# Optimization experiments

Measured on AMD Instinct MI355X. Metric: run time of the kernel, lower is better.

## Reference

```python
import jax, jax.numpy as jnp
import numpy as np

NL, D, DI, N, R, K = 4, 256, 512, 16, 16, 4  # layers, d_model, d_inner, d_state, dt_rank, conv kernel


def setup_inputs() -> dict:
    key = jax.random.key(0)
    ks = jax.random.split(key, 10)
    b, nc, nt = 8, 256, 64
    xc = jax.random.normal(ks[0], (b, nc, D), jnp.float32)
    xt = jax.random.normal(ks[1], (b, nt, D), jnp.float32)
    ln_g = jnp.ones((NL, D), jnp.float32)
    ln_b = jnp.zeros((NL, D), jnp.float32)
    W_in = jax.random.normal(ks[2], (NL, D, 2 * DI), jnp.float32) * (D ** -0.5)
    W_conv = jax.random.normal(ks[3], (NL, DI, 1, K), jnp.float32) * 0.2
    b_conv = jnp.zeros((NL, DI), jnp.float32)
    W_x = jax.random.normal(ks[4], (NL, DI, R + 2 * N), jnp.float32) * (DI ** -0.5)
    W_dt = jax.random.normal(ks[5], (NL, R, DI), jnp.float32) * (R ** -0.5)
    b_dt = jax.random.normal(ks[6], (NL, DI), jnp.float32) * 0.5 - 4.0  # softplus ~ 0.02
    A_log = jnp.broadcast_to(jnp.log(jnp.arange(1, N + 1, dtype=jnp.float32)), (NL, DI, N)).copy()
    Dp = jnp.ones((NL, DI), jnp.float32)
    W_out = jax.random.normal(ks[7], (NL, DI, D), jnp.float32) * (DI ** -0.5)
    return dict(xc=xc, xt=xt, ln_g=ln_g, ln_b=ln_b, W_in=W_in, W_conv=W_conv, b_conv=b_conv,
                W_x=W_x, W_dt=W_dt, b_dt=b_dt, A_log=A_log, Dp=Dp, W_out=W_out)


def _mamba_layer(x, g, beta, Wi, Wc, bc, Wx, Wdt, bdt, Alog, Dvec, Wo):
    # x: [B, L, D]; pre-LN residual Mamba-1 block
    mu = jnp.mean(x, axis=-1, keepdims=True)
    var = jnp.var(x, axis=-1, keepdims=True)
    h = (x - mu) * jax.lax.rsqrt(var + 1e-5) * g + beta
    xz = h @ Wi                              # [B, L, 2*DI]
    xp, z = xz[..., :DI], xz[..., DI:]
    # causal depthwise conv1d
    xcv = jax.lax.conv_general_dilated(xp.transpose(0, 2, 1), Wc, (1,), [(K - 1, 0)],
                                       feature_group_count=DI,
                                       dimension_numbers=('NCH', 'OIH', 'NCH'))
    xcv = jax.nn.silu(xcv.transpose(0, 2, 1) + bc)  # [B, L, DI]
    dbl = xcv @ Wx                           # [B, L, R+2N]
    dt = jax.nn.softplus(dbl[..., :R] @ Wdt + bdt)   # [B, L, DI]
    Bm = dbl[..., R:R + N]                   # [B, L, N]
    Cm = dbl[..., R + N:]                    # [B, L, N]
    A = -jnp.exp(Alog)                       # [DI, N]

    def step(hst, inp):
        x_t, dt_t, b_t, c_t = inp            # [B,DI],[B,DI],[B,N],[B,N]
        dA = jnp.exp(dt_t[:, :, None] * A)   # [B, DI, N]
        hst = dA * hst + (dt_t * x_t)[:, :, None] * b_t[:, None, :]
        return hst, jnp.einsum('bdn,bn->bd', hst, c_t)

    h0 = jnp.zeros((x.shape[0], DI, N), x.dtype)
    _, ys = jax.lax.scan(step, h0, (xcv.transpose(1, 0, 2), dt.transpose(1, 0, 2),
                                    Bm.transpose(1, 0, 2), Cm.transpose(1, 0, 2)))
    y = ys.transpose(1, 0, 2) + xcv * Dvec
    y = y * jax.nn.silu(z)
    return x + y @ Wo


def reference(xc, xt, ln_g, ln_b, W_in, W_conv, b_conv, W_x, W_dt, b_dt, A_log, Dp, W_out):
    b, nc, d = xc.shape
    nt = xt.shape[1]
    # replicate context per target token: [b*nt, nc+1, d]
    xr = jnp.broadcast_to(xc[:, None], (b, nt, nc, d)).reshape(b * nt, nc, d)
    x = jnp.concatenate([xr, xt.reshape(b * nt, 1, d)], axis=1)
    for i in range(NL):
        x = _mamba_layer(x, ln_g[i], ln_b[i], W_in[i], W_conv[i], b_conv[i],
                         W_x[i], W_dt[i], b_dt[i], A_log[i], Dp[i], W_out[i])
    return x[:, -1, :].reshape(b, nt, d)
```

## Files before the change

### kernel.cpp

```cpp
#include <hip/hip_runtime.h>
#include <hip/hip_bf16.h>

#define D_     256
#define TWO_DI 1024
#define DI_    512
#define NSTATE 16
#define RR     16
#define NDBL   48
#define BSEQ   8
#define NC     256
#define NCHUNK 16
#define CLEN   16
#define CTX    2048
#define TGT    512

typedef __attribute__((ext_vector_type(8))) short short8v;
typedef __attribute__((ext_vector_type(8))) unsigned short ushort8v;
typedef __attribute__((ext_vector_type(4))) float floatx4;

__device__ __forceinline__ float siluf(float x) { return x / (1.f + __expf(-x)); }
__device__ __forceinline__ float softplusf(float x) {
  return fmaxf(x, 0.f) + log1pf(__expf(-fabsf(x)));
}
__device__ __forceinline__ unsigned short f2bf(float x) {
  unsigned u = __float_as_uint(x);
  u += 0x7fffu + ((u >> 16) & 1u);
  return (unsigned short)(u >> 16);
}
__device__ __forceinline__ float bf2f(unsigned short b) {
  return __uint_as_float((unsigned)b << 16);
}

__global__ __launch_bounds__(256) void prep_all(
    const float* __restrict__ W_in, const float* __restrict__ W_o,
    const float* __restrict__ W_x, const float* __restrict__ Alog,
    unsigned short* __restrict__ Wint, unsigned short* __restrict__ Wot,
    unsigned short* __restrict__ Wxt, float* __restrict__ Aneg)
{
  __shared__ float tile[32][33];
  int b = blockIdx.x;
  const float* src; unsigned short* dst; int R, C, cx, ry;
  if (b < 1024) {
    int z = b >> 8, t = b & 255; cx = t & 31; ry = t >> 5; R = 256; C = 1024;
    src = W_in + (size_t)z * R * C; dst = Wint + (size_t)z * R * C;
  } else if (b < 1536) {
    int bb = b - 1024; int z = bb >> 7, t = bb & 127; cx = t & 7; ry = t >> 3; R = 512; C = 256;
    src = W_o + (size_t)z * R * C; dst = Wot + (size_t)z * R * C;
  } else if (b < 1664) {
    int bb = b - 1536; int z = bb >> 5, t = bb & 31; cx = t & 1; ry = t >> 1; R = 512; C = 48;
    src = W_x + (size_t)z * R * C; dst = Wxt + (size_t)z * R * C;
  } else {
    int i = (b - 1664) * 256 + threadIdx.x;
    if (i < 4 * DI_ * NSTATE) Aneg[i] = -__expf(Alog[i]);
    return;
  }
  int c0 = cx * 32, r0 = ry * 32;
  int tx = threadIdx.x & 31, ty = threadIdx.x >> 5;
#pragma unroll
  for (int i = 0; i < 4; ++i) {
    int r = r0 + ty + i * 8;
    tile[ty + i * 8][tx] = (r < R && c0 + tx < C) ? src[(size_t)r * C + c0 + tx] : 0.f;
  }
  __syncthreads();
#pragma unroll
  for (int i = 0; i < 4; ++i) {
    int c = c0 + ty + i * 8;
    if (c < C && r0 + tx < R)
      dst[(size_t)c * R + r0 + tx] = f2bf(tile[tx][ty + i * 8]);
  }
}

__device__ __forceinline__ void ln_body(int bx, const float* __restrict__ x,
    const float* __restrict__ g, const float* __restrict__ be,
    unsigned short* __restrict__ out, int rows)
{
  int wid = threadIdx.x >> 6, lane = threadIdx.x & 63;
  int row = bx * 4 + wid;
  if (row >= rows) return;
  const float4 v = *reinterpret_cast<const float4*>(&x[(size_t)row * D_ + lane * 4]);
  float s  = v.x + v.y + v.z + v.w;
  float sq = v.x * v.x + v.y * v.y + v.z * v.z + v.w * v.w;
#pragma unroll
  for (int off = 32; off; off >>= 1) {
    s  += __shfl_xor(s, off);
    sq += __shfl_xor(sq, off);
  }
  float mu   = s * (1.f / D_);
  float var  = sq * (1.f / D_) - mu * mu;
  float rstd = rsqrtf(var + 1e-5f);
  const float4 gv = *reinterpret_cast<const float4*>(&g[lane * 4]);
  const float4 bv = *reinterpret_cast<const float4*>(&be[lane * 4]);
  ushort4 o;
  o.x = f2bf((v.x - mu) * rstd * gv.x + bv.x);
  o.y = f2bf((v.y - mu) * rstd * gv.y + bv.y);
  o.z = f2bf((v.z - mu) * rstd * gv.z + bv.z);
  o.w = f2bf((v.w - mu) * rstd * gv.w + bv.w);
  *reinterpret_cast<ushort4*>(&out[(size_t)row * D_ + lane * 4]) = o;
}

__global__ __launch_bounds__(256) void ln_kern(const float* __restrict__ x,
    const float* __restrict__ g, const float* __restrict__ be,
    unsigned short* __restrict__ out, int rows)
{
  ln_body(blockIdx.x, x, g, be, out, rows);
}

__global__ __launch_bounds__(256) void fused_ln(
    const float* __restrict__ xA, const float* __restrict__ gA,
    const float* __restrict__ bA, unsigned short* __restrict__ oA,
    const float* __restrict__ xB, const float* __restrict__ gB,
    const float* __restrict__ bB, unsigned short* __restrict__ oB)
{
  if (blockIdx.x < CTX / 4) ln_body(blockIdx.x, xA, gA, bA, oA, CTX);
  else                      ln_body(blockIdx.x - CTX / 4, xB, gB, bB, oB, TGT);
}

template<int EPI>
__device__ __forceinline__ void gemm_body(
    unsigned short (*As)[72], unsigned short (*Bs)[72], int bx, int by,
    const unsigned short* __restrict__ A, const unsigned short* __restrict__ Bt,
    const float* __restrict__ resid, float* __restrict__ C, int M, int N, int K,
    const float* __restrict__ cconv, const float* __restrict__ Wc4,
    unsigned short* __restrict__ xcv_bf, float* __restrict__ zbuf)
{
  int tid = threadIdx.x;
  int n0 = bx * 64, m0 = by * 64;
  int w = tid >> 6, lane = tid & 63;
  int lr = lane & 15, kq = lane >> 4;
  int wr = w >> 1, wc = w & 1;
  int srow = tid >> 2, schunk = (tid & 3) * 16;
  const unsigned short* Ap = &A[(size_t)(m0 + srow) * K + schunk];
  const unsigned short* Bp = &Bt[(size_t)(n0 + srow) * K + schunk];
  ushort8v a0 = *reinterpret_cast<const ushort8v*>(Ap);
  ushort8v a1 = *reinterpret_cast<const ushort8v*>(Ap + 8);
  ushort8v b0 = *reinterpret_cast<const ushort8v*>(Bp);
  ushort8v b1 = *reinterpret_cast<const ushort8v*>(Bp + 8);
  floatx4 acc[2][2] = {};
  for (int k0 = 0; k0 < K; k0 += 64) {
    __syncthreads();
    *reinterpret_cast<ushort8v*>(&As[srow][schunk])     = a0;
    *reinterpret_cast<ushort8v*>(&As[srow][schunk + 8]) = a1;
    *reinterpret_cast<ushort8v*>(&Bs[srow][schunk])     = b0;
    *reinterpret_cast<ushort8v*>(&Bs[srow][schunk + 8]) = b1;
    __syncthreads();
    if (k0 + 64 < K) {
      a0 = *reinterpret_cast<const ushort8v*>(Ap + k0 + 64);
      a1 = *reinterpret_cast<const ushort8v*>(Ap + k0 + 72);
      b0 = *reinterpret_cast<const ushort8v*>(Bp + k0 + 64);
      b1 = *reinterpret_cast<const ushort8v*>(Bp + k0 + 72);
    }
#pragma unroll
    for (int ks = 0; ks < 2; ++ks) {
      short8v af[2], bf2v[2];
#pragma unroll
      for (int f = 0; f < 2; ++f)
        af[f] = *reinterpret_cast<const short8v*>(&As[wr * 32 + f * 16 + lr][ks * 32 + kq * 8]);
#pragma unroll
      for (int g2 = 0; g2 < 2; ++g2)
        bf2v[g2] = *reinterpret_cast<const short8v*>(&Bs[wc * 32 + g2 * 16 + lr][ks * 32 + kq * 8]);
#pragma unroll
      for (int f = 0; f < 2; ++f)
#pragma unroll
        for (int g2 = 0; g2 < 2; ++g2)
          acc[f][g2] = __builtin_amdgcn_mfma_f32_16x16x32_bf16(af[f], bf2v[g2], acc[f][g2], 0, 0, 0);
    }
  }
#pragma unroll
  for (int f = 0; f < 2; ++f)
#pragma unroll
    for (int g2 = 0; g2 < 2; ++g2) {
      int col = n0 + wc * 32 + g2 * 16 + lr;
#pragma unroll
      for (int r = 0; r < 4; ++r) {
        int row = m0 + wr * 32 + f * 16 + kq * 4 + r;
        float v = acc[f][g2][r];
        if (EPI == 0) {
          if (resid) v += resid[(size_t)row * N + col];
          C[(size_t)row * N + col] = v;
        } else {
          int b = row >> 6;
          if (col < DI_) {
            float sv = siluf(cconv[b * DI_ + col] + v * Wc4[col * 4 + 3]);
            xcv_bf[(size_t)row * DI_ + col] = f2bf(sv);
          } else {
            zbuf[(size_t)row * DI_ + (col - DI_)] = v;
          }
        }
      }
    }
}

template<int EPI>
__global__ __launch_bounds__(256) void gemm_bf16(
    const unsigned short* __restrict__ A, const unsigned short* __restrict__ Bt,
    const float* __restrict__ resid, float* __restrict__ C, int M, int N, int K,
    const float* __restrict__ cconv, const float* __restrict__ Wc4,
    unsigned short* __restrict__ xcv_bf, float* __restrict__ zbuf)
{
  __shared__ unsigned short As[64][72];
  __shared__ unsigned short Bs[64][72];
  gemm_body<EPI>(As, Bs, blockIdx.x, blockIdx.y, A, Bt, resid, C, M, N, K,
                 cconv, Wc4, xcv_bf, zbuf);
}

__global__ __launch_bounds__(256) void fused_gemm_in(
    const unsigned short* __restrict__ Aa, const unsigned short* __restrict__ Bta,
    float* __restrict__ Ca,
    const unsigned short* __restrict__ Ab, const unsigned short* __restrict__ Btb,
    const float* __restrict__ cconv, const float* __restrict__ Wc4,
    unsigned short* __restrict__ xcv_bf, float* __restrict__ zbuf)
{
  __shared__ unsigned short As[64][72];
  __shared__ unsigned short Bs[64][72];
  int f = blockIdx.x;
  if (f < 512)
    gemm_body<0>(As, Bs, f & 15, f >> 4, Aa, Bta, nullptr, Ca, CTX, TWO_DI, D_,
                 nullptr, nullptr, nullptr, nullptr);
  else {
    f -= 512;
    gemm_body<1>(As, Bs, f & 15, f >> 4, Ab, Btb, nullptr, nullptr, TGT, TWO_DI, D_,
                 cconv, Wc4, xcv_bf, zbuf);
  }
}

__device__ __forceinline__ void gemm_s_body(int bx, int by,
    const unsigned short* __restrict__ A, const unsigned short* __restrict__ Bt,
    const float* __restrict__ resid, float* __restrict__ C, int M, int N, int K)
{
  __shared__ unsigned short As[32][72];
  __shared__ unsigned short Bs[32][72];
  int tid = threadIdx.x;
  int n0 = bx * 32, m0 = by * 32;
  int w = tid >> 6, lane = tid & 63;
  int lr = lane & 15, kq = lane >> 4;
  int wr = w >> 1, wc = w & 1;
  int srow = tid >> 3, schunk = (tid & 7) * 8;
  const unsigned short* Ap = &A[(size_t)(m0 + srow) * K + schunk];
  const unsigned short* Bp = &Bt[(size_t)(n0 + srow) * K + schunk];
  ushort8v a0 = *reinterpret_cast<const ushort8v*>(Ap);
  ushort8v b0 = *reinterpret_cast<const ushort8v*>(Bp);
  floatx4 acc = {};
  for (int k0 = 0; k0 < K; k0 += 64) {
    __syncthreads();
    *reinterpret_cast<ushort8v*>(&As[srow][schunk]) = a0;
    *reinterpret_cast<ushort8v*>(&Bs[srow][schunk]) = b0;
    __syncthreads();
    if (k0 + 64 < K) {
      a0 = *reinterpret_cast<const ushort8v*>(Ap + k0 + 64);
      b0 = *reinterpret_cast<const ushort8v*>(Bp + k0 + 64);
    }
#pragma unroll
    for (int ks = 0; ks < 2; ++ks) {
      short8v af = *reinterpret_cast<const short8v*>(&As[wr * 16 + lr][ks * 32 + kq * 8]);
      short8v bf = *reinterpret_cast<const short8v*>(&Bs[wc * 16 + lr][ks * 32 + kq * 8]);
      acc = __builtin_amdgcn_mfma_f32_16x16x32_bf16(af, bf, acc, 0, 0, 0);
    }
  }
  int col = n0 + wc * 16 + lr;
#pragma unroll
  for (int r = 0; r < 4; ++r) {
    int row = m0 + wr * 16 + kq * 4 + r;
    float v = acc[r];
    if (resid) v += resid[(size_t)row * N + col];
    C[(size_t)row * N + col] = v;
  }
}

__global__ __launch_bounds__(256) void gemm_s(
    const unsigned short* __restrict__ A, const unsigned short* __restrict__ Bt,
    const float* __restrict__ resid, float* __restrict__ C, int M, int N, int K)
{
  gemm_s_body(blockIdx.x, blockIdx.y, A, Bt, resid, C, M, N, K);
}

__device__ __forceinline__ void conv_body(int blk,
    const float* __restrict__ xz, const float* __restrict__ Wc,
    const float* __restrict__ bc, const unsigned short* __restrict__ Wxt,
    const float* __restrict__ Wdt, const float* __restrict__ bdt,
    const float* __restrict__ Aneg,
    unsigned short* __restrict__ xcvb, float* __restrict__ dtb,
    float* __restrict__ dblg, float* __restrict__ cconv,
    float* __restrict__ Sb, float* __restrict__ Pb)
{
  __shared__ unsigned short xcs[16][528];
  __shared__ float dts_s[16][520];
  __shared__ float dbl_s[16][48];
  int seq = blk >> 4, ch = blk & 15;
  int tok0 = blk * 16;
  int tid = threadIdx.x;
#pragma unroll
  for (int hh = 0; hh < 2; ++hh) {
    int c = tid + hh * 256;
    float w0 = Wc[c * 4 + 0], w1 = Wc[c * 4 + 1], w2 = Wc[c * 4 + 2], w3 = Wc[c * 4 + 3];
    float bcv = bc[c];
    const float* xzs = &xz[(size_t)(seq * NC) * TWO_DI + c];
    for (int t = 0; t < 16; ++t) {
      int tl = ch * 16 + t;
      float acc = bcv + xzs[(size_t)tl * TWO_DI] * w3;
      if (tl >= 1) acc += xzs[(size_t)(tl - 1) * TWO_DI] * w2;
      if (tl >= 2) acc += xzs[(size_t)(tl - 2) * TWO_DI] * w1;
      if (tl >= 3) acc += xzs[(size_t)(tl - 3) * TWO_DI] * w0;
      unsigned short sv = f2bf(siluf(acc));
      xcs[t][c] = sv;
      xcvb[(size_t)(tok0 + t) * DI_ + c] = sv;
    }
    if (ch == 15)
      cconv[seq * DI_ + c] = bcv + xzs[(size_t)253 * TWO_DI] * w0
                                 + xzs[(size_t)254 * TWO_DI] * w1
                                 + xzs[(size_t)255 * TWO_DI] * w2;
  }
  __syncthreads();
  int w = tid >> 6, lane = tid & 63, lr = lane & 15, kq = lane >> 4;
  if (w < 3) {
    floatx4 acc = {};
#pragma unroll
    for (int kc = 0; kc < 16; ++kc) {
      short8v bb = *reinterpret_cast<const short8v*>(&Wxt[(size_t)(w * 16 + lr) * DI_ + kc * 32 + kq * 8]);
      short8v aa = *reinterpret_cast<const short8v*>(&xcs[lr][kc * 32 + kq * 8]);
      acc = __builtin_amdgcn_mfma_f32_16x16x32_bf16(aa, bb, acc, 0, 0, 0);
    }
#pragma unroll
    for (int r = 0; r < 4; ++r) {
      int t = kq * 4 + r, col = w * 16 + lr;
      dbl_s[t][col] = acc[r];
      dblg[(size_t)(tok0 + t) * NDBL + col] = acc[r];
    }
  }
  __syncthreads();
#pragma unroll
  for (int hh = 0; hh < 2; ++hh) {
    int c = tid + hh * 256;
    float wr_[16];
#pragma unroll
    for (int r = 0; r < 16; ++r) wr_[r] = Wdt[r * DI_ + c];
    float bv = bdt[c];
    for (int t = 0; t < 16; ++t) {
      float accd = bv;
#pragma unroll
      for (int r = 0; r < 16; ++r) accd += dbl_s[t][r] * wr_[r];
      float dtv = softplusf(accd);
      dts_s[t][c] = dtv;
      dtb[(size_t)(tok0 + t) * DI_ + c] = dtv;
    }
  }
  __syncthreads();
  int dl = tid >> 4, n = tid & 15;
  float Bt_r[16];
#pragma unroll
  for (int t = 0; t < 16; ++t) Bt_r[t] = dbl_s[t][RR + n];
  for (int dg = 0; dg < 32; ++dg) {
    int d = dg * 16 + dl;
    float A = Aneg[d * NSTATE + n];
    float h = 0.f, p = 1.f;
#pragma unroll
    for (int t = 0; t < 16; ++t) {
      float dtv = dts_s[t][d];
      float xv  = bf2f(xcs[t][d]);
      float dA  = __expf(dtv * A);
      h = fmaf(dA, h, dtv * xv * Bt_r[t]);
      p *= dA;
    }
    size_t o = ((size_t)blk * DI_ + d) * NSTATE + n;
    Sb[o] = h; Pb[o] = p;
  }
}

__global__ __launch_bounds__(256) void conv_dbl_part(
    const float* __restrict__ xz, const float* __restrict__ Wc,
    const float* __restrict__ bc, const unsigned short* __restrict__ Wxt,
    const float* __restrict__ Wdt, const float* __restrict__ bdt,
    const float* __restrict__ Aneg,
    unsigned short* __restrict__ xcvb, float* __restrict__ dtb,
    float* __restrict__ dblg, float* __restrict__ cconv,
    float* __restrict__ Sb, float* __restrict__ Pb)
{
  conv_body(blockIdx.x, xz, Wc, bc, Wxt, Wdt, bdt, Aneg, xcvb, dtb, dblg, cconv, Sb, Pb);
}

__device__ __forceinline__ void sf_body(int b,
    const float* __restrict__ dblg, const unsigned short* __restrict__ xcvb,
    const float* __restrict__ xz, const float* __restrict__ dtb,
    const float* __restrict__ Sb, const float* __restrict__ Pb,
    const float* __restrict__ Aneg, const float* __restrict__ Dp,
    unsigned short* __restrict__ yb, float* __restrict__ hstate)
{
  int dg = b & 31, sc = b >> 5;
  int seq = sc >> 4, chunk = sc & 15;
  int tid = threadIdx.x;
  int tt = tid >> 4, cc = tid & 15;
  int tok0 = sc * CLEN;
  __shared__ float dts[16][17], xs[16][17], zs[16][17], Bs[16][17], Cs[16][17], ys[16][17];
  dts[tt][cc] = dtb[(size_t)(tok0 + tt) * DI_ + dg * 16 + cc];
  xs[tt][cc]  = bf2f(xcvb[(size_t)(tok0 + tt) * DI_ + dg * 16 + cc]);
  zs[tt][cc]  = xz[(size_t)(tok0 + tt) * TWO_DI + DI_ + dg * 16 + cc];
  Bs[tt][cc]  = dblg[(size_t)(tok0 + tt) * NDBL + RR + cc];
  Cs[tt][cc]  = dblg[(size_t)(tok0 + tt) * NDBL + RR + NSTATE + cc];
  __syncthreads();
  int dl = tt, n = cc;
  int d = dg * 16 + dl;
  float A  = Aneg[d * NSTATE + n];
  float Dv = Dp[d];
  float Bn[16], Cn[16];
#pragma unroll
  for (int t = 0; t < CLEN; ++t) { Bn[t] = Bs[t][n]; Cn[t] = Cs[t][n]; }
  float h = 0.f;
  for (int c2 = 0; c2 < chunk; ++c2) {
    size_t o = ((size_t)(seq * NCHUNK + c2) * DI_ + d) * NSTATE + n;
    h = fmaf(Pb[o], h, Sb[o]);
  }
#pragma unroll
  for (int t = 0; t < CLEN; ++t) {
    float dtv = dts[t][dl];
    float xv  = xs[t][dl];
    float dA  = __expf(dtv * A);
    h = fmaf(dA, h, dtv * xv * Bn[t]);
    float p = h * Cn[t];
    p += __shfl_xor(p, 1); p += __shfl_xor(p, 2);
    p += __shfl_xor(p, 4); p += __shfl_xor(p, 8);
    if (n == 0) ys[t][dl] = (p + xv * Dv) * siluf(zs[t][dl]);
  }
  __syncthreads();
  yb[(size_t)(tok0 + tt) * DI_ + dg * 16 + cc] = f2bf(ys[tt][cc]);
  if (chunk == NCHUNK - 1)
    hstate[(size_t)seq * DI_ * NSTATE + d * NSTATE + n] = h;
}

__global__ __launch_bounds__(256) void scan_fin(
    const float* __restrict__ dblg, const unsigned short* __restrict__ xcvb,
    const float* __restrict__ xz, const float* __restrict__ dtb,
    const float* __restrict__ Sb, const float* __restrict__ Pb,
    const float* __restrict__ Aneg, const float* __restrict__ Dp,
    unsigned short* __restrict__ yb, float* __restrict__ hstate)
{
  sf_body(blockIdx.x, dblg, xcvb, xz, dtb, Sb, Pb, Aneg, Dp, yb, hstate);
}

__device__ __forceinline__ void ssm_body(int blk,
    const unsigned short* __restrict__ xcv_bf, const float* __restrict__ zbuf,
    const unsigned short* __restrict__ Wx, const float* __restrict__ Wdt_l,
    const float* __restrict__ bdt_l, const float* __restrict__ An_l,
    const float* __restrict__ Dp_l, const float* __restrict__ hs,
    unsigned short* __restrict__ ybf)
{
  __shared__ float dbl_s[16][48];
  int tg = blk >> 3, cg = blk & 7;
  int tok0 = tg * 16;
  int b = tg >> 2;
  int tid = threadIdx.x;
  int w = tid >> 6, lane = tid & 63, lr = lane & 15, kq = lane >> 4;
  if (w < 3) {
    floatx4 acc = {};
#pragma unroll
    for (int kc = 0; kc < 16; ++kc) {
      short8v bb = *reinterpret_cast<const short8v*>(&Wx[(size_t)(w * 16 + lr) * DI_ + kc * 32 + kq * 8]);
      short8v aa = *reinterpret_cast<const short8v*>(&xcv_bf[(size_t)(tok0 + lr) * DI_ + kc * 32 + kq * 8]);
      acc = __builtin_amdgcn_mfma_f32_16x16x32_bf16(aa, bb, acc, 0, 0, 0);
    }
#pragma unroll
    for (int r = 0; r < 4; ++r)
      dbl_s[kq * 4 + r][w * 16 + lr] = acc[r];
  }
  __syncthreads();
  int c = cg * 64 + (tid & 63);
  int t0 = (tid >> 6) * 4;
  float wdt_r[16], An[16], hr[16];
#pragma unroll
  for (int r = 0; r < 16; ++r) wdt_r[r] = Wdt_l[r * DI_ + c];
  const float4* An4 = reinterpret_cast<const float4*>(&An_l[c * NSTATE]);
  const float4* hr4 = reinterpret_cast<const float4*>(&hs[(size_t)b * DI_ * NSTATE + c * NSTATE]);
#pragma unroll
  for (int q = 0; q < 4; ++q) {
    float4 a = An4[q]; An[q*4]=a.x; An[q*4+1]=a.y; An[q*4+2]=a.z; An[q*4+3]=a.w;
    float4 hv = hr4[q]; hr[q*4]=hv.x; hr[q*4+1]=hv.y; hr[q*4+2]=hv.z; hr[q*4+3]=hv.w;
  }
  float Dv = Dp_l[c], bv = bdt_l[c];
#pragma unroll
  for (int tt = 0; tt < 4; ++tt) {
    int t = t0 + tt;
    float accd = bv;
#pragma unroll
    for (int r = 0; r < 16; ++r) accd += dbl_s[t][r] * wdt_r[r];
    float dtv = softplusf(accd);
    float xv = bf2f(xcv_bf[(size_t)(tok0 + t) * DI_ + c]);
    float coef = dtv * xv;
    float y = 0.f;
#pragma unroll
    for (int n = 0; n < 16; ++n) {
      float hn = fmaf(__expf(dtv * An[n]), hr[n], coef * dbl_s[t][RR + n]);
      y = fmaf(hn, dbl_s[t][RR + NSTATE + n], y);
    }
    float yv = (y + xv * Dv) * siluf(zbuf[(size_t)(tok0 + t) * DI_ + c]);
    ybf[(size_t)(tok0 + t) * DI_ + c] = f2bf(yv);
  }
}

__global__ __launch_bounds__(256) void tgt_ssm2(
    const unsigned short* __restrict__ xcv_bf, const float* __restrict__ zbuf,
    const unsigned short* __restrict__ Wx, const float* __restrict__ Wdt_l,
    const float* __restrict__ bdt_l, const float* __restrict__ An_l,
    const float* __restrict__ Dp_l, const float* __restrict__ hs,
    unsigned short* __restrict__ ybf)
{
  ssm_body(blockIdx.x, xcv_bf, zbuf, Wx, Wdt_l, bdt_l, An_l, Dp_l, hs, ybf);
}

__global__ __launch_bounds__(256) void fused_conv_ssm(
    const float* __restrict__ xz, const float* __restrict__ Wc,
    const float* __restrict__ bc, const unsigned short* __restrict__ WxtA,
    const float* __restrict__ WdtA, const float* __restrict__ bdtA,
    const float* __restrict__ AnegA,
    unsigned short* __restrict__ xcvb, float* __restrict__ dtb,
    float* __restrict__ dblg, float* __restrict__ cconv,
    float* __restrict__ Sb, float* __restrict__ Pb,
    const unsigned short* __restrict__ xcv_bfB, const float* __restrict__ zbufB,
    const unsigned short* __restrict__ WxB, const float* __restrict__ WdtB,
    const float* __restrict__ bdtB, const float* __restrict__ AnB,
    const float* __restrict__ DpB, const float* __restrict__ hsB,
    unsigned short* __restrict__ ybfB)
{
  if (blockIdx.x < BSEQ * NCHUNK)
    conv_body(blockIdx.x, xz, Wc, bc, WxtA, WdtA, bdtA, AnegA,
              xcvb, dtb, dblg, cconv, Sb, Pb);
  else
    ssm_body(blockIdx.x - BSEQ * NCHUNK, xcv_bfB, zbufB, WxB, WdtB, bdtB,
             AnB, DpB, hsB, ybfB);
}

__global__ __launch_bounds__(256) void fused_sf_gout(
    const unsigned short* __restrict__ Ag, const unsigned short* __restrict__ Btg,
    const float* __restrict__ residg, float* __restrict__ Cg,
    const float* __restrict__ dblg, const unsigned short* __restrict__ xcvb,
    const float* __restrict__ xz, const float* __restrict__ dtb,
    const float* __restrict__ Sb, const float* __restrict__ Pb,
    const float* __restrict__ Aneg, const float* __restrict__ Dp,
    unsigned short* __restrict__ yb, float* __restrict__ hstate)
{
  if (blockIdx.x < 128) {
    int f = blockIdx.x;
    gemm_s_body(f & 7, f >> 3, Ag, Btg, residg, Cg, TGT, D_, DI_);
  } else {
    sf_body(blockIdx.x - 128, dblg, xcvb, xz, dtb, Sb, Pb, Aneg, Dp, yb, hstate);
  }
}

extern "C" void kernel_launch(void* const* d_in, const int* in_sizes, int n_in,
                              void* d_out, int out_size, void* d_ws, size_t ws_size,
                              hipStream_t stream)
{
  const float* xc   = (const float*)d_in[0];
  const float* xt   = (const float*)d_in[1];
  const float* ln_g = (const float*)d_in[2];
  const float* ln_b = (const float*)d_in[3];
  const float* W_in = (const float*)d_in[4];
  const float* W_cv = (const float*)d_in[5];
  const float* b_cv = (const float*)d_in[6];
  const float* W_x  = (const float*)d_in[7];
  const float* W_dt = (const float*)d_in[8];
  const float* b_dt = (const float*)d_in[9];
  const float* Alog = (const float*)d_in[10];
  const float* Dp   = (const float*)d_in[11];
  const float* W_o  = (const float*)d_in[12];
  float* out = (float*)d_out;

  float* ws = (float*)d_ws;
  size_t off = 0;
  auto alloc = [&](size_t n) { float* p = ws + off; off += n; return p; };
  float* xz     = alloc((size_t)CTX * TWO_DI);
  float* dtb    = alloc((size_t)CTX * DI_);
  float* dblg   = alloc((size_t)CTX * NDBL);
  float* xcur   = alloc((size_t)CTX * D_);
  float* Sb     = alloc((size_t)BSEQ * NCHUNK * DI_ * NSTATE);
  float* Pb     = alloc((size_t)BSEQ * NCHUNK * DI_ * NSTATE);
  float* cconvT = alloc((size_t)4 * BSEQ * DI_);
  float* hst    = alloc((size_t)4 * BSEQ * DI_ * NSTATE);
  float* Aneg   = alloc((size_t)4 * DI_ * NSTATE);
  float* zbufB  = alloc((size_t)TGT * DI_);
  float* xtb    = alloc((size_t)TGT * D_);
  unsigned short* hbuf_bf = (unsigned short*)alloc((size_t)CTX * D_ / 2);
  unsigned short* hbufB   = (unsigned short*)alloc((size_t)TGT * D_ / 2);
  unsigned short* xcvb    = (unsigned short*)alloc((size_t)CTX * DI_ / 2);
  unsigned short* yb_bf   = (unsigned short*)alloc((size_t)CTX * DI_ / 2);
  unsigned short* xcv_bfB = (unsigned short*)alloc((size_t)TGT * DI_ / 2);
  unsigned short* y_bfB   = (unsigned short*)alloc((size_t)TGT * DI_ / 2);
  unsigned short* Wint    = (unsigned short*)alloc((size_t)4 * TWO_DI * D_ / 2);
  unsigned short* Wot     = (unsigned short*)alloc((size_t)4 * D_ * DI_ / 2);
  unsigned short* Wxt     = (unsigned short*)alloc((size_t)4 * NDBL * DI_ / 2);
  if (off * sizeof(float) > ws_size) return;

  prep_all<<<1792, 256, 0, stream>>>(W_in, W_o, W_x, Alog, Wint, Wot, Wxt, Aneg);

  ln_kern<<<CTX / 4, 256, 0, stream>>>(xc, ln_g, ln_b, hbuf_bf, CTX);
  gemm_bf16<0><<<dim3(TWO_DI / 64, CTX / 64), 256, 0, stream>>>(
      hbuf_bf, Wint, nullptr, xz, CTX, TWO_DI, D_, nullptr, nullptr, nullptr, nullptr);
  conv_dbl_part<<<BSEQ * NCHUNK, 256, 0, stream>>>(
      xz, W_cv, b_cv, Wxt, W_dt, b_dt, Aneg, xcvb, dtb, dblg, cconvT, Sb, Pb);
  scan_fin<<<BSEQ * NCHUNK * 32, 256, 0, stream>>>(
      dblg, xcvb, xz, dtb, Sb, Pb, Aneg, Dp, yb_bf, hst);
  gemm_bf16<0><<<dim3(D_ / 64, CTX / 64), 256, 0, stream>>>(
      yb_bf, Wot, xc, xcur, CTX, D_, DI_, nullptr, nullptr, nullptr, nullptr);

  for (int l = 0; l < 3; ++l) {
    int la = l + 1;
    const float* xinB = (l == 0) ? xt : xtb;
    fused_ln<<<CTX / 4 + TGT / 4, 256, 0, stream>>>(
        xcur, ln_g + la * D_, ln_b + la * D_, hbuf_bf,
        xinB, ln_g + l * D_,  ln_b + l * D_,  hbufB);
    fused_gemm_in<<<512 + 128, 256, 0, stream>>>(
        hbuf_bf, Wint + (size_t)la * TWO_DI * D_, xz,
        hbufB,   Wint + (size_t)l * TWO_DI * D_,
        cconvT + (size_t)l * BSEQ * DI_, W_cv + l * DI_ * 4, xcv_bfB, zbufB);
    fused_conv_ssm<<<BSEQ * NCHUNK + 256, 256, 0, stream>>>(
        xz, W_cv + la * DI_ * 4, b_cv + la * DI_, Wxt + (size_t)la * NDBL * DI_,
        W_dt + la * RR * DI_, b_dt + la * DI_, Aneg + la * DI_ * NSTATE,
        xcvb, dtb, dblg, cconvT + (size_t)la * BSEQ * DI_, Sb, Pb,
        xcv_bfB, zbufB, Wxt + (size_t)l * NDBL * DI_, W_dt + l * RR * DI_,
        b_dt + l * DI_, Aneg + l * DI_ * NSTATE, Dp + l * DI_,
        hst + (size_t)l * BSEQ * DI_ * NSTATE, y_bfB);
    fused_sf_gout<<<128 + BSEQ * NCHUNK * 32, 256, 0, stream>>>(
        y_bfB, Wot + (size_t)l * D_ * DI_, xinB, xtb,
        dblg, xcvb, xz, dtb, Sb, Pb, Aneg + la * DI_ * NSTATE, Dp + la * DI_,
        yb_bf, hst + (size_t)la * BSEQ * DI_ * NSTATE);
    if (la < 3)
      gemm_bf16<0><<<dim3(D_ / 64, CTX / 64), 256, 0, stream>>>(
          yb_bf, Wot + (size_t)la * D_ * DI_, xcur, xcur, CTX, D_, DI_,
          nullptr, nullptr, nullptr, nullptr);
  }

  ln_kern<<<TGT / 4, 256, 0, stream>>>(xtb, ln_g + 3 * D_, ln_b + 3 * D_, hbufB, TGT);
  gemm_bf16<1><<<dim3(TWO_DI / 64, TGT / 64), 256, 0, stream>>>(
      hbufB, Wint + (size_t)3 * TWO_DI * D_, nullptr, nullptr, TGT, TWO_DI, D_,
      cconvT + (size_t)3 * BSEQ * DI_, W_cv + 3 * DI_ * 4, xcv_bfB, zbufB);
  tgt_ssm2<<<256, 256, 0, stream>>>(xcv_bfB, zbufB,
      Wxt + (size_t)3 * NDBL * DI_, W_dt + 3 * RR * DI_, b_dt + 3 * DI_,
      Aneg + 3 * DI_ * NSTATE, Dp + 3 * DI_,
      hst + (size_t)3 * BSEQ * DI_ * NSTATE, y_bfB);
  gemm_s<<<dim3(D_ / 32, TGT / 32), 256, 0, stream>>>(
      y_bfB, Wot + (size_t)3 * D_ * DI_, xtb, out, TGT, D_, DI_);
}
```

Baseline: 360.3 us.

## Split chunk-partial scan out of conv kernel into a widely parallel kernel

Moves the per-chunk SSM partial-state scan (Sb/Pb) out of the 128-block conv kernel into its own 4096-block kernel, or fuses it with the output GEMM, so that work is spread across many more CUs instead of serialized inside a few blocks. The conv stage also gets a register sliding window for the depthwise conv and reads a pre-transposed W_dt with float4 loads. In exchange, the later stage of each layer now runs as an extra scan_fin launch rather than being fused with the output GEMM, and dt/xcv are round-tripped through global memory.

```diff
diff --git a/kernel.cpp b/kernel.cpp
--- a/kernel.cpp
+++ b/kernel.cpp
@@ -34,8 +34,10 @@
 __global__ __launch_bounds__(256) void prep_all(
     const float* __restrict__ W_in, const float* __restrict__ W_o,
     const float* __restrict__ W_x, const float* __restrict__ Alog,
+    const float* __restrict__ W_dt,
     unsigned short* __restrict__ Wint, unsigned short* __restrict__ Wot,
-    unsigned short* __restrict__ Wxt, float* __restrict__ Aneg)
+    unsigned short* __restrict__ Wxt, float* __restrict__ Aneg,
+    float* __restrict__ WdtT)
 {
   __shared__ float tile[32][33];
   int b = blockIdx.x;
@@ -49,9 +51,14 @@
   } else if (b < 1664) {
     int bb = b - 1536; int z = bb >> 5, t = bb & 31; cx = t & 1; ry = t >> 1; R = 512; C = 48;
     src = W_x + (size_t)z * R * C; dst = Wxt + (size_t)z * R * C;
-  } else {
+  } else if (b < 1792) {
     int i = (b - 1664) * 256 + threadIdx.x;
     if (i < 4 * DI_ * NSTATE) Aneg[i] = -__expf(Alog[i]);
+    return;
+  } else {
+    int i = (b - 1792) * 256 + threadIdx.x;
+    int z = i >> 13, rem = i & 8191, c = rem >> 4, r = rem & 15;
+    WdtT[i] = W_dt[(size_t)z * RR * DI_ + r * DI_ + c];
     return;
   }
   int c0 = cx * 32, r0 = ry * 32;
@@ -273,41 +280,40 @@
   gemm_s_body(blockIdx.x, blockIdx.y, A, Bt, resid, C, M, N, K);
 }
 
-__device__ __forceinline__ void conv_body(int blk,
+__device__ __forceinline__ void conv_body_lean(int blk,
     const float* __restrict__ xz, const float* __restrict__ Wc,
     const float* __restrict__ bc, const unsigned short* __restrict__ Wxt,
-    const float* __restrict__ Wdt, const float* __restrict__ bdt,
-    const float* __restrict__ Aneg,
+    const float* __restrict__ WdtT, const float* __restrict__ bdt,
     unsigned short* __restrict__ xcvb, float* __restrict__ dtb,
-    float* __restrict__ dblg, float* __restrict__ cconv,
-    float* __restrict__ Sb, float* __restrict__ Pb)
+    float* __restrict__ dblg, float* __restrict__ cconv)
 {
   __shared__ unsigned short xcs[16][528];
-  __shared__ float dts_s[16][520];
   __shared__ float dbl_s[16][48];
   int seq = blk >> 4, ch = blk & 15;
   int tok0 = blk * 16;
   int tid = threadIdx.x;
+  int base = ch * 16;
 #pragma unroll
   for (int hh = 0; hh < 2; ++hh) {
     int c = tid + hh * 256;
-    float w0 = Wc[c * 4 + 0], w1 = Wc[c * 4 + 1], w2 = Wc[c * 4 + 2], w3 = Wc[c * 4 + 3];
+    const float4 wv = *reinterpret_cast<const float4*>(&Wc[c * 4]);
     float bcv = bc[c];
     const float* xzs = &xz[(size_t)(seq * NC) * TWO_DI + c];
+    float r[19];
+#pragma unroll
+    for (int i = 0; i < 19; ++i) {
+      int tl = base - 3 + i;
+      r[i] = (tl >= 0) ? xzs[(size_t)tl * TWO_DI] : 0.f;
+    }
+#pragma unroll
     for (int t = 0; t < 16; ++t) {
-      int tl = ch * 16 + t;
-      float acc = bcv + xzs[(size_t)tl * TWO_DI] * w3;
-      if (tl >= 1) acc += xzs[(size_t)(tl - 1) * TWO_DI] * w2;
-      if (tl >= 2) acc += xzs[(size_t)(tl - 2) * TWO_DI] * w1;
-      if (tl >= 3) acc += xzs[(size_t)(tl - 3) * TWO_DI] * w0;
+      float acc = bcv + r[t] * wv.x + r[t + 1] * wv.y + r[t + 2] * wv.z + r[t + 3] * wv.w;
       unsigned short sv = f2bf(siluf(acc));
       xcs[t][c] = sv;
       xcvb[(size_t)(tok0 + t) * DI_ + c] = sv;
     }
     if (ch == 15)
-      cconv[seq * DI_ + c] = bcv + xzs[(size_t)253 * TWO_DI] * w0
-                                 + xzs[(size_t)254 * TWO_DI] * w1
-                                 + xzs[(size_t)255 * TWO_DI] * w2;
+      cconv[seq * DI_ + c] = bcv + r[16] * wv.x + r[17] * wv.y + r[18] * wv.z;
   }
   __syncthreads();
   int w = tid >> 6, lane = tid & 63, lr = lane & 15, kq = lane >> 4;
@@ -320,10 +326,10 @@
       acc = __builtin_amdgcn_mfma_f32_16x16x32_bf16(aa, bb, acc, 0, 0, 0);
     }
 #pragma unroll
-    for (int r = 0; r < 4; ++r) {
-      int t = kq * 4 + r, col = w * 16 + lr;
-      dbl_s[t][col] = acc[r];
-      dblg[(size_t)(tok0 + t) * NDBL + col] = acc[r];
+    for (int r2 = 0; r2 < 4; ++r2) {
+      int t = kq * 4 + r2, col = w * 16 + lr;
+      dbl_s[t][col] = acc[r2];
+      dblg[(size_t)(tok0 + t) * NDBL + col] = acc[r2];
     }
   }
   __syncthreads();
@@ -331,59 +337,96 @@
   for (int hh = 0; hh < 2; ++hh) {
     int c = tid + hh * 256;
     float wr_[16];
-#pragma unroll
-    for (int r = 0; r < 16; ++r) wr_[r] = Wdt[r * DI_ + c];
+    const float4* wt4 = reinterpret_cast<const float4*>(&WdtT[c * 16]);
+#pragma unroll
+    for (int q = 0; q < 4; ++q) {
+      float4 v4 = wt4[q];
+      wr_[q * 4] = v4.x; wr_[q * 4 + 1] = v4.y; wr_[q * 4 + 2] = v4.z; wr_[q * 4 + 3] = v4.w;
+    }
     float bv = bdt[c];
+#pragma unroll
     for (int t = 0; t < 16; ++t) {
       float accd = bv;
 #pragma unroll
-      for (int r = 0; r < 16; ++r) accd += dbl_s[t][r] * wr_[r];
-      float dtv = softplusf(accd);
-      dts_s[t][c] = dtv;
-      dtb[(size_t)(tok0 + t) * DI_ + c] = dtv;
-    }
-  }
-  __syncthreads();
-  int dl = tid >> 4, n = tid & 15;
-  float Bt_r[16];
-#pragma unroll
-  for (int t = 0; t < 16; ++t) Bt_r[t] = dbl_s[t][RR + n];
-  for (int dg = 0; dg < 32; ++dg) {
-    int d = dg * 16 + dl;
-    float A = Aneg[d * NSTATE + n];
-    float h = 0.f, p = 1.f;
-#pragma unroll
-    for (int t = 0; t < 16; ++t) {
-      float dtv = dts_s[t][d];
-      float xv  = bf2f(xcs[t][d]);
-      float dA  = __expf(dtv * A);
-      h = fmaf(dA, h, dtv * xv * Bt_r[t]);
-      p *= dA;
-    }
-    size_t o = ((size_t)blk * DI_ + d) * NSTATE + n;
-    Sb[o] = h; Pb[o] = p;
-  }
-}
-
-__global__ __launch_bounds__(256) void conv_dbl_part(
+      for (int r2 = 0; r2 < 16; ++r2) accd += dbl_s[t][r2] * wr_[r2];
+      dtb[(size_t)(tok0 + t) * DI_ + c] = softplusf(accd);
+    }
+  }
+}
+
+__global__ __launch_bounds__(256) void conv_lean_kern(
     const float* __restrict__ xz, const float* __restrict__ Wc,
     const float* __restrict__ bc, const unsigned short* __restrict__ Wxt,
-    const float* __restrict__ Wdt, const float* __restrict__ bdt,
-    const float* __restrict__ Aneg,
+    const float* __restrict__ WdtT, const float* __restrict__ bdt,
     unsigned short* __restrict__ xcvb, float* __restrict__ dtb,
-    float* __restrict__ dblg, float* __restrict__ cconv,
+    float* __restrict__ dblg, float* __restrict__ cconv)
+{
+  conv_body_lean(blockIdx.x, xz, Wc, bc, Wxt, WdtT, bdt, xcvb, dtb, dblg, cconv);
+}
+
+__device__ __forceinline__ void sp_body(int b,
+    const float* __restrict__ dblg, const unsigned short* __restrict__ xcvb,
+    const float* __restrict__ dtb, const float* __restrict__ Aneg,
     float* __restrict__ Sb, float* __restrict__ Pb)
 {
-  conv_body(blockIdx.x, xz, Wc, bc, Wxt, Wdt, bdt, Aneg, xcvb, dtb, dblg, cconv, Sb, Pb);
-}
-
-__device__ __forceinline__ void sf_body(int b,
+  int dg = b & 31, sc = b >> 5;
+  int tid = threadIdx.x;
+  int tt = tid >> 4, cc = tid & 15;
+  int tok0 = sc * CLEN;
+  __shared__ float dts[16][17], xs[16][17], Bs[16][17];
+  dts[tt][cc] = dtb[(size_t)(tok0 + tt) * DI_ + dg * 16 + cc];
+  xs[tt][cc]  = bf2f(xcvb[(size_t)(tok0 + tt) * DI_ + dg * 16 + cc]);
+  Bs[tt][cc]  = dblg[(size_t)(tok0 + tt) * NDBL + RR + cc];
+  __syncthreads();
+  int dl = tt, n = cc;
+  int d = dg * 16 + dl;
+  float A = Aneg[d * NSTATE + n];
+  float Bn[16];
+#pragma unroll
+  for (int t = 0; t < CLEN; ++t) Bn[t] = Bs[t][n];
+  float h = 0.f, p = 1.f;
+#pragma unroll
+  for (int t = 0; t < CLEN; ++t) {
+    float dtv = dts[t][dl];
+    float dA  = __expf(dtv * A);
+    h = fmaf(dA, h, dtv * xs[t][dl] * Bn[t]);
+    p *= dA;
+  }
+  size_t o = ((size_t)sc * DI_ + d) * NSTATE + n;
+  Sb[o] = h; Pb[o] = p;
+}
+
+__global__ __launch_bounds__(256) void sp_kern(
+    const float* __restrict__ dblg, const unsigned short* __restrict__ xcvb,
+    const float* __restrict__ dtb, const float* __restrict__ Aneg,
+    float* __restrict__ Sb, float* __restrict__ Pb)
+{
+  sp_body(blockIdx.x, dblg, xcvb, dtb, Aneg, Sb, Pb);
+}
+
+__global__ __launch_bounds__(256) void fused_sp_gout(
+    const unsigned short* __restrict__ Ag, const unsigned short* __restrict__ Btg,
+    const float* __restrict__ residg, float* __restrict__ Cg,
+    const float* __restrict__ dblg, const unsigned short* __restrict__ xcvb,
+    const float* __restrict__ dtb, const float* __restrict__ Aneg,
+    float* __restrict__ Sb, float* __restrict__ Pb)
+{
+  if (blockIdx.x < 128) {
+    int f = blockIdx.x;
+    gemm_s_body(f & 7, f >> 3, Ag, Btg, residg, Cg, TGT, D_, DI_);
+  } else {
+    sp_body(blockIdx.x - 128, dblg, xcvb, dtb, Aneg, Sb, Pb);
+  }
+}
+
+__global__ __launch_bounds__(256) void scan_fin(
     const float* __restrict__ dblg, const unsigned short* __restrict__ xcvb,
     const float* __restrict__ xz, const float* __restrict__ dtb,
     const float* __restrict__ Sb, const float* __restrict__ Pb,
     const float* __restrict__ Aneg, const float* __restrict__ Dp,
     unsigned short* __restrict__ yb, float* __restrict__ hstate)
 {
+  int b = blockIdx.x;
   int dg = b & 31, sc = b >> 5;
   int seq = sc >> 4, chunk = sc & 15;
   int tid = threadIdx.x;
@@ -425,19 +468,9 @@
     hstate[(size_t)seq * DI_ * NSTATE + d * NSTATE + n] = h;
 }
 
-__global__ __launch_bounds__(256) void scan_fin(
-    const float* __restrict__ dblg, const unsigned short* __restrict__ xcvb,
-    const float* __restrict__ xz, const float* __restrict__ dtb,
-    const float* __restrict__ Sb, const float* __restrict__ Pb,
-    const float* __restrict__ Aneg, const float* __restrict__ Dp,
-    unsigned short* __restrict__ yb, float* __restrict__ hstate)
-{
-  sf_body(blockIdx.x, dblg, xcvb, xz, dtb, Sb, Pb, Aneg, Dp, yb, hstate);
-}
-
 __device__ __forceinline__ void ssm_body(int blk,
     const unsigned short* __restrict__ xcv_bf, const float* __restrict__ zbuf,
-    const unsigned short* __restrict__ Wx, const float* __restrict__ Wdt_l,
+    const unsigned short* __restrict__ Wx, const float* __restrict__ WdtT_l,
     const float* __restrict__ bdt_l, const float* __restrict__ An_l,
     const float* __restrict__ Dp_l, const float* __restrict__ hs,
     unsigned short* __restrict__ ybf)
@@ -464,12 +497,12 @@
   int c = cg * 64 + (tid & 63);
   int t0 = (tid >> 6) * 4;
   float wdt_r[16], An[16], hr[16];
-#pragma unroll
-  for (int r = 0; r < 16; ++r) wdt_r[r] = Wdt_l[r * DI_ + c];
+  const float4* wt4 = reinterpret_cast<const float4*>(&WdtT_l[c * 16]);
   const float4* An4 = reinterpret_cast<const float4*>(&An_l[c * NSTATE]);
   const float4* hr4 = reinterpret_cast<const float4*>(&hs[(size_t)b * DI_ * NSTATE + c * NSTATE]);
 #pragma unroll
   for (int q = 0; q < 4; ++q) {
+    float4 wv = wt4[q]; wdt_r[q*4]=wv.x; wdt_r[q*4+1]=wv.y; wdt_r[q*4+2]=wv.z; wdt_r[q*4+3]=wv.w;
     float4 a = An4[q]; An[q*4]=a.x; An[q*4+1]=a.y; An[q*4+2]=a.z; An[q*4+3]=a.w;
     float4 hv = hr4[q]; hr[q*4]=hv.x; hr[q*4+1]=hv.y; hr[q*4+2]=hv.z; hr[q*4+3]=hv.w;
   }
@@ -496,51 +529,32 @@
 
 __global__ __launch_bounds__(256) void tgt_ssm2(
     const unsigned short* __restrict__ xcv_bf, const float* __restrict__ zbuf,
-    const unsigned short* __restrict__ Wx, const float* __restrict__ Wdt_l,
+    const unsigned short* __restrict__ Wx, const float* __restrict__ WdtT_l,
     const float* __restrict__ bdt_l, const float* __restrict__ An_l,
     const float* __restrict__ Dp_l, const float* __restrict__ hs,
     unsigned short* __restrict__ ybf)
 {
-  ssm_body(blockIdx.x, xcv_bf, zbuf, Wx, Wdt_l, bdt_l, An_l, Dp_l, hs, ybf);
+  ssm_body(blockIdx.x, xcv_bf, zbuf, Wx, WdtT_l, bdt_l, An_l, Dp_l, hs, ybf);
 }
 
 __global__ __launch_bounds__(256) void fused_conv_ssm(
     const float* __restrict__ xz, const float* __restrict__ Wc,
     const float* __restrict__ bc, const unsigned short* __restrict__ WxtA,
-    const float* __restrict__ WdtA, const float* __restrict__ bdtA,
-    const float* __restrict__ AnegA,
+    const float* __restrict__ WdtTA, const float* __restrict__ bdtA,
     unsigned short* __restrict__ xcvb, float* __restrict__ dtb,
     float* __restrict__ dblg, float* __restrict__ cconv,
-    float* __restrict__ Sb, float* __restrict__ Pb,
     const unsigned short* __restrict__ xcv_bfB, const float* __restrict__ zbufB,
-    const unsigned short* __restrict__ WxB, const float* __restrict__ WdtB,
+    const unsigned short* __restrict__ WxB, const float* __restrict__ WdtTB,
     const float* __restrict__ bdtB, const float* __restrict__ AnB,
     const float* __restrict__ DpB, const float* __restrict__ hsB,
     unsigned short* __restrict__ ybfB)
 {
   if (blockIdx.x < BSEQ * NCHUNK)
-    conv_body(blockIdx.x, xz, Wc, bc, WxtA, WdtA, bdtA, AnegA,
-              xcvb, dtb, dblg, cconv, Sb, Pb);
+    conv_body_lean(blockIdx.x, xz, Wc, bc, WxtA, WdtTA, bdtA,
+                   xcvb, dtb, dblg, cconv);
   else
-    ssm_body(blockIdx.x - BSEQ * NCHUNK, xcv_bfB, zbufB, WxB, WdtB, bdtB,
+    ssm_body(blockIdx.x - BSEQ * NCHUNK, xcv_bfB, zbufB, WxB, WdtTB, bdtB,
              AnB, DpB, hsB, ybfB);
-}
-
-__global__ __launch_bounds__(256) void fused_sf_gout(
-    const unsigned short* __restrict__ Ag, const unsigned short* __restrict__ Btg,
-    const float* __restrict__ residg, float* __restrict__ Cg,
-    const float* __restrict__ dblg, const unsigned short* __restrict__ xcvb,
-    const float* __restrict__ xz, const float* __restrict__ dtb,
-    const float* __restrict__ Sb, const float* __restrict__ Pb,
-    const float* __restrict__ Aneg, const float* __restrict__ Dp,
-    unsigned short* __restrict__ yb, float* __restrict__ hstate)
-{
-  if (blockIdx.x < 128) {
-    int f = blockIdx.x;
-    gemm_s_body(f & 7, f >> 3, Ag, Btg, residg, Cg, TGT, D_, DI_);
-  } else {
-    sf_body(blockIdx.x - 128, dblg, xcvb, xz, dtb, Sb, Pb, Aneg, Dp, yb, hstate);
-  }
 }
 
 extern "C" void kernel_launch(void* const* d_in, const int* in_sizes, int n_in,
@@ -574,6 +588,7 @@
   float* cconvT = alloc((size_t)4 * BSEQ * DI_);
   float* hst    = alloc((size_t)4 * BSEQ * DI_ * NSTATE);
   float* Aneg   = alloc((size_t)4 * DI_ * NSTATE);
+  float* WdtT   = alloc((size_t)4 * DI_ * RR);
   float* zbufB  = alloc((size_t)TGT * DI_);
   float* xtb    = alloc((size_t)TGT * D_);
   unsigned short* hbuf_bf = (unsigned short*)alloc((size_t)CTX * D_ / 2);
@@ -587,13 +602,15 @@
   unsigned short* Wxt     = (unsigned short*)alloc((size_t)4 * NDBL * DI_ / 2);
   if (off * sizeof(float) > ws_size) return;
 
-  prep_all<<<1792, 256, 0, stream>>>(W_in, W_o, W_x, Alog, Wint, Wot, Wxt, Aneg);
+  prep_all<<<1920, 256, 0, stream>>>(W_in, W_o, W_x, Alog, W_dt,
+                                     Wint, Wot, Wxt, Aneg, WdtT);
 
   ln_kern<<<CTX / 4, 256, 0, stream>>>(xc, ln_g, ln_b, hbuf_bf, CTX);
   gemm_bf16<0><<<dim3(TWO_DI / 64, CTX / 64), 256, 0, stream>>>(
       hbuf_bf, Wint, nullptr, xz, CTX, TWO_DI, D_, nullptr, nullptr, nullptr, nullptr);
-  conv_dbl_part<<<BSEQ * NCHUNK, 256, 0, stream>>>(
-      xz, W_cv, b_cv, Wxt, W_dt, b_dt, Aneg, xcvb, dtb, dblg, cconvT, Sb, Pb);
+  conv_lean_kern<<<BSEQ * NCHUNK, 256, 0, stream>>>(
+      xz, W_cv, b_cv, Wxt, WdtT, b_dt, xcvb, dtb, dblg, cconvT);
+  sp_kern<<<BSEQ * NCHUNK * 32, 256, 0, stream>>>(dblg, xcvb, dtb, Aneg, Sb, Pb);
   scan_fin<<<BSEQ * NCHUNK * 32, 256, 0, stream>>>(
       dblg, xcvb, xz, dtb, Sb, Pb, Aneg, Dp, yb_bf, hst);
   gemm_bf16<0><<<dim3(D_ / 64, CTX / 64), 256, 0, stream>>>(
@@ -611,13 +628,15 @@
         cconvT + (size_t)l * BSEQ * DI_, W_cv + l * DI_ * 4, xcv_bfB, zbufB);
     fused_conv_ssm<<<BSEQ * NCHUNK + 256, 256, 0, stream>>>(
         xz, W_cv + la * DI_ * 4, b_cv + la * DI_, Wxt + (size_t)la * NDBL * DI_,
-        W_dt + la * RR * DI_, b_dt + la * DI_, Aneg + la * DI_ * NSTATE,
-        xcvb, dtb, dblg, cconvT + (size_t)la * BSEQ * DI_, Sb, Pb,
-        xcv_bfB, zbufB, Wxt + (size_t)l * NDBL * DI_, W_dt + l * RR * DI_,
+        WdtT + (size_t)la * DI_ * RR, b_dt + la * DI_,
+        xcvb, dtb, dblg, cconvT + (size_t)la * BSEQ * DI_,
+        xcv_bfB, zbufB, Wxt + (size_t)l * NDBL * DI_, WdtT + (size_t)l * DI_ * RR,
         b_dt + l * DI_, Aneg + l * DI_ * NSTATE, Dp + l * DI_,
         hst + (size_t)l * BSEQ * DI_ * NSTATE, y_bfB);
-    fused_sf_gout<<<128 + BSEQ * NCHUNK * 32, 256, 0, stream>>>(
+    fused_sp_gout<<<128 + BSEQ * NCHUNK * 32, 256, 0, stream>>>(
         y_bfB, Wot + (size_t)l * D_ * DI_, xinB, xtb,
+        dblg, xcvb, dtb, Aneg + la * DI_ * NSTATE, Sb, Pb);
+    scan_fin<<<BSEQ * NCHUNK * 32, 256, 0, stream>>>(
         dblg, xcvb, xz, dtb, Sb, Pb, Aneg + la * DI_ * NSTATE, Dp + la * DI_,
         yb_bf, hst + (size_t)la * BSEQ * DI_ * NSTATE);
     if (la < 3)
@@ -631,7 +650,7 @@
       hbufB, Wint + (size_t)3 * TWO_DI * D_, nullptr, nullptr, TGT, TWO_DI, D_,
       cconvT + (size_t)3 * BSEQ * DI_, W_cv + 3 * DI_ * 4, xcv_bfB, zbufB);
   tgt_ssm2<<<256, 256, 0, stream>>>(xcv_bfB, zbufB,
-      Wxt + (size_t)3 * NDBL * DI_, W_dt + 3 * RR * DI_, b_dt + 3 * DI_,
+      Wxt + (size_t)3 * NDBL * DI_, WdtT + (size_t)3 * DI_ * RR, b_dt + 3 * DI_,
       Aneg + 3 * DI_ * NSTATE, Dp + 3 * DI_,
       hst + (size_t)3 * BSEQ * DI_ * NSTATE, y_bfB);
   gemm_s<<<dim3(D_ / 32, TGT / 32), 256, 0, stream>>>(
```

New measurement: 306.3 us. 15.0% less time.
